# Performance work log

Measured on AMD Instinct MI355X. Metric: run time of the kernel, lower is better.

Reference implementation:

```python
import jax, jax.numpy as jnp
import numpy as np

T, B, C, H = 2048, 2, 1024, 16
D = C // H
SCALE = D ** -0.5
WSTD = C ** -0.5  # keep activations O(1) so softmax is not saturated


def setup_inputs() -> dict:
    key = jax.random.key(0)
    ks = jax.random.split(key, 6)
    return {
        "x": jax.random.normal(ks[0], (T, B, C), dtype=jnp.float32),
        "wq": jax.random.normal(ks[1], (C, C), dtype=jnp.float32) * WSTD,
        "wk": jax.random.normal(ks[2], (C, C), dtype=jnp.float32) * WSTD,
        "wv": jax.random.normal(ks[3], (C, C), dtype=jnp.float32) * WSTD,
        "wo": jax.random.normal(ks[4], (C, C), dtype=jnp.float32) * WSTD,
        "bo": jax.random.normal(ks[5], (C,), dtype=jnp.float32) * 0.02,
    }


def reference(x, wq, wk, wv, wo, bo):
    t, b, c = x.shape
    x2 = x.reshape(t * b, c)
    # SelfAttentionLinears: q scaled by head_dim^-0.5 inside the addmm
    q = (x2 @ wq) * SCALE
    k = x2 @ wk
    v = x2 @ wv
    # fairseq layout: (T, B*H, D) -> (B*H, T, D)
    q = q.reshape(t, b * H, D).transpose(1, 0, 2)
    k = k.reshape(t, b * H, D).transpose(1, 0, 2)
    v = v.reshape(t, b * H, D).transpose(1, 0, 2)
    # strided_bmm1: scores [B*H, T, T]
    scores = jnp.einsum('bqd,bkd->bqk', q, k)
    attn = jax.nn.softmax(scores, axis=-1)
    # strided_bmm2: context [B*H, T, D]
    ctx = jnp.einsum('bqk,bkd->bqd', attn, v)
    out = ctx.transpose(1, 0, 2).reshape(t, b, c)
    return out @ wo + bo
```

## Files before the change

kernel.cpp:

```cpp
#include <hip/hip_runtime.h>
#include <math.h>

#define T_DIM 2048
#define B_DIM 2
#define C_DIM 1024
#define H_DIM 16
#define D_DIM 64
#define M_DIM (T_DIM * B_DIM)
#define SCALE_QL2 0.18033688f

typedef short short8 __attribute__((ext_vector_type(8)));
typedef float f32x4  __attribute__((ext_vector_type(4)));
typedef unsigned short ushort_t;

__device__ __forceinline__ unsigned short f2bf(float f) {
    unsigned int u = __builtin_bit_cast(unsigned int, f);
    u += 0x7FFFu + ((u >> 16) & 1u);
    return (unsigned short)(u >> 16);
}

__device__ __forceinline__ void gl_lds16(const void* g, void* l) {
    __builtin_amdgcn_global_load_lds(
        (const __attribute__((address_space(1))) void*)g,
        (__attribute__((address_space(3))) void*)l, 16, 0, 0);
}

__global__ __launch_bounds__(256) void prep(
    const float* __restrict__ x,
    const float* __restrict__ wq, const float* __restrict__ wk,
    const float* __restrict__ wv, const float* __restrict__ wo,
    ushort_t* __restrict__ xb,
    ushort_t* __restrict__ wqkv_t, ushort_t* __restrict__ wo_t)
{
    __shared__ float tile[64][65];
    const int tid = threadIdx.x;
    const int z   = blockIdx.z;

    if (z == 4) {
        const size_t base =
            ((size_t)(blockIdx.y * 16 + blockIdx.x)) * 16384 + (size_t)tid * 8;
#pragma unroll
        for (int j = 0; j < 8; ++j) {
            const size_t i = base + (size_t)j * 2048;
            const float4 v0 = *(const float4*)&x[i];
            const float4 v1 = *(const float4*)&x[i + 4];
            ushort_t o[8] = {f2bf(v0.x), f2bf(v0.y), f2bf(v0.z), f2bf(v0.w),
                             f2bf(v1.x), f2bf(v1.y), f2bf(v1.z), f2bf(v1.w)};
            *(uint4*)&xb[i] = *(uint4*)o;
        }
        return;
    }

    const int k0 = blockIdx.x * 64;
    const int n0 = blockIdx.y * 64;
    const float* src = (z == 0) ? wq : (z == 1) ? wk : (z == 2) ? wv : wo;
    ushort_t* dst = (z < 3) ? (wqkv_t + (size_t)z * C_DIM * C_DIM) : wo_t;

    const int r = tid >> 4;
    const int c = (tid & 15) * 4;
#pragma unroll
    for (int i = 0; i < 4; ++i) {
        const float4 v = *(const float4*)&src[(size_t)(k0 + r + i * 16) * C_DIM + n0 + c];
        *(float4*)&tile[r + i * 16][c] = v;
    }
    __syncthreads();
#pragma unroll
    for (int i = 0; i < 4; ++i) {
        const int r2 = r + i * 16;
        ushort4 o;
        o.x = f2bf(tile[c + 0][r2]); o.y = f2bf(tile[c + 1][r2]);
        o.z = f2bf(tile[c + 2][r2]); o.w = f2bf(tile[c + 3][r2]);
        *(ushort4*)&dst[(size_t)(n0 + r2) * C_DIM + k0 + c] = o;
    }
}

__global__ __launch_bounds__(256) void qkv_mfma(
    const ushort_t* __restrict__ xb, const ushort_t* __restrict__ wt,
    ushort_t* __restrict__ q_ws, ushort_t* __restrict__ k_ws,
    ushort_t* __restrict__ v_ws)
{
    __shared__ ushort_t lds[18432];
    ushort_t* As = lds;
    ushort_t* Bs = lds + 4096;

    const int tid  = threadIdx.x;
    const int n0   = blockIdx.x * 128;
    const int m0   = blockIdx.y * 128;
    const int w    = tid >> 6;
    const int lane = tid & 63;
    const int l16  = lane & 15;
    const int quad = lane >> 4;
    const int wm   = (w >> 1) * 64;
    const int wn   = (w & 1) * 64;

    const int o0 = tid * 8, o1 = o0 + 2048;
    const ushort_t* a0 = xb + (size_t)(m0 + (o0 >> 5)) * C_DIM + (o0 & 31);
    const ushort_t* a1 = xb + (size_t)(m0 + (o1 >> 5)) * C_DIM + (o1 & 31);
    const ushort_t* b0 = wt + (size_t)(n0 + (o0 >> 5)) * C_DIM + (o0 & 31);
    const ushort_t* b1 = wt + (size_t)(n0 + (o1 >> 5)) * C_DIM + (o1 & 31);

    f32x4 acc[4][4] = {};

    for (int k0 = 0; k0 < C_DIM; k0 += 32) {
        __syncthreads();
        gl_lds16(a0 + k0, As + o0);
        gl_lds16(a1 + k0, As + o1);
        gl_lds16(b0 + k0, Bs + o0);
        gl_lds16(b1 + k0, Bs + o1);
        __syncthreads();

        short8 af[4], bf[4];
#pragma unroll
        for (int mi = 0; mi < 4; ++mi)
            af[mi] = *(const short8*)&As[(wm + mi * 16 + l16) * 32 + quad * 8];
#pragma unroll
        for (int ni = 0; ni < 4; ++ni)
            bf[ni] = *(const short8*)&Bs[(wn + ni * 16 + l16) * 32 + quad * 8];
#pragma unroll
        for (int mi = 0; mi < 4; ++mi)
#pragma unroll
            for (int ni = 0; ni < 4; ++ni)
                acc[mi][ni] = __builtin_amdgcn_mfma_f32_16x16x32_bf16(
                    af[mi], bf[ni], acc[mi][ni], 0, 0, 0);
    }

    __syncthreads();
    ushort_t* Ep = lds + w * 4608;

    const int mat = n0 >> 10;
    const int cb  = (n0 & 1023) + wn;
    const int h   = cb >> 6;
    ushort_t* dst = (mat == 0) ? q_ws : (mat == 1) ? k_ws : v_ws;
    const float sc = (mat == 0) ? SCALE_QL2 : 1.0f;

#pragma unroll
    for (int mi = 0; mi < 4; ++mi)
#pragma unroll
        for (int ni = 0; ni < 4; ++ni)
#pragma unroll
            for (int r = 0; r < 4; ++r)
                Ep[(mi * 16 + quad * 4 + r) * 72 + ni * 16 + l16] =
                    f2bf(acc[mi][ni][r] * sc);

    const int rq = lane >> 3;
    const int c8 = (lane & 7) * 8;
#pragma unroll
    for (int p = 0; p < 8; ++p) {
        const int row = p * 8 + rq;
        const uint4 val = *(const uint4*)&Ep[row * 72 + c8];
        const int m = m0 + wm + row;
        const int t = m >> 1, b = m & 1;
        *(uint4*)&dst[((size_t)(b * H_DIM + h) * T_DIM + t) * D_DIM + c8] = val;
    }
}

__global__ __launch_bounds__(256) void v_transpose(
    const ushort_t* __restrict__ vn, ushort_t* __restrict__ vt)
{
    __shared__ ushort_t tile[64][72];
    const int tid = threadIdx.x;
    const int t0  = blockIdx.x * 64;
    const int bh  = blockIdx.y;
    const int r   = tid >> 3;
    const int c   = (tid & 7) * 8;
#pragma unroll
    for (int i = 0; i < 2; ++i)
        *(uint4*)&tile[r + i * 32][c] =
            *(const uint4*)&vn[((size_t)bh * T_DIM + t0 + r + i * 32) * D_DIM + c];
    __syncthreads();
#pragma unroll
    for (int i = 0; i < 2; ++i) {
        const int rd = r + i * 32;
        ushort_t o[8];
#pragma unroll
        for (int j = 0; j < 8; ++j) o[j] = tile[c + j][rd];
        *(uint4*)&vt[((size_t)bh * D_DIM + rd) * T_DIM + t0 + c] = *(uint4*)o;
    }
}

__global__ __launch_bounds__(256) void attn_mfma(
    const ushort_t* __restrict__ q, const ushort_t* __restrict__ k,
    const ushort_t* __restrict__ v, ushort_t* __restrict__ ctx)
{
    __shared__ ushort_t Ks [64][72];
    __shared__ ushort_t Vts[64][72];
    __shared__ ushort_t Ps [64][72];

    const int tid  = threadIdx.x;
    const int bh   = blockIdx.x;
    const int q0   = blockIdx.y * 64;
    const int w    = tid >> 6;
    const int lane = tid & 63;
    const int l16  = lane & 15;
    const int quad = lane >> 4;

    const int r0 = tid >> 3,         c80 = (tid & 7) * 8;
    const int r1 = (tid + 256) >> 3;
    const ushort_t* kbase = k + (size_t)bh * T_DIM * D_DIM;
    const ushort_t* vbase = v + (size_t)bh * D_DIM * T_DIM;

    short8 aq0, aq1;
    {
        const ushort_t* qrow = q + ((size_t)bh * T_DIM + q0 + 16 * w + l16) * D_DIM;
        aq0 = *(const short8*)(qrow + quad * 8);
        aq1 = *(const short8*)(qrow + 32 + quad * 8);
    }

    short8 vones;
#pragma unroll
    for (int j = 0; j < 8; ++j) vones[j] = (short)0x3F80;

    f32x4 O[4] = {};
    f32x4 Osum = {};

    const ushort_t* kp0 = kbase + (size_t)r0 * D_DIM + c80;
    const ushort_t* kp1 = kbase + (size_t)r1 * D_DIM + c80;
    const ushort_t* vp0 = vbase + (size_t)r0 * T_DIM + c80;
    const ushort_t* vp1 = vbase + (size_t)r1 * T_DIM + c80;
    uint4 kr0 = *(const uint4*)kp0;  kp0 += 64 * D_DIM;
    uint4 kr1 = *(const uint4*)kp1;  kp1 += 64 * D_DIM;
    uint4 vr0 = *(const uint4*)vp0;  vp0 += 64;
    uint4 vr1 = *(const uint4*)vp1;  vp1 += 64;

    for (int kt = 0; kt < 32; ++kt) {
        __syncthreads();
        *(uint4*)&Ks[r0][c80]  = kr0;
        *(uint4*)&Ks[r1][c80]  = kr1;
        *(uint4*)&Vts[r0][c80] = vr0;
        *(uint4*)&Vts[r1][c80] = vr1;
        if (kt + 1 < 32) {
            kr0 = *(const uint4*)kp0;  kp0 += 64 * D_DIM;
            kr1 = *(const uint4*)kp1;  kp1 += 64 * D_DIM;
            vr0 = *(const uint4*)vp0;  vp0 += 64;
            vr1 = *(const uint4*)vp1;  vp1 += 64;
        }
        __syncthreads();

        f32x4 S[4];
        __builtin_amdgcn_s_setprio(1);
#pragma unroll
        for (int nt = 0; nt < 4; ++nt) {
            const short8 b0 = *(const short8*)&Ks[nt * 16 + l16][quad * 8];
            const short8 b1 = *(const short8*)&Ks[nt * 16 + l16][32 + quad * 8];
            f32x4 s = (f32x4){0.f, 0.f, 0.f, 0.f};
            s = __builtin_amdgcn_mfma_f32_16x16x32_bf16(aq0, b0, s, 0, 0, 0);
            s = __builtin_amdgcn_mfma_f32_16x16x32_bf16(aq1, b1, s, 0, 0, 0);
            S[nt] = s;
        }
        __builtin_amdgcn_s_setprio(0);

#pragma unroll
        for (int nt = 0; nt < 4; ++nt)
#pragma unroll
            for (int r = 0; r < 4; ++r) {
                union { float f; ushort2 h; } cv;
                cv.f = exp2f(S[nt][r]);
                Ps[16 * w + quad * 4 + r][nt * 16 + l16] = cv.h.y;
            }

        const short8 ap0 = *(const short8*)&Ps[16 * w + l16][quad * 8];
        const short8 ap1 = *(const short8*)&Ps[16 * w + l16][32 + quad * 8];

        __builtin_amdgcn_s_setprio(1);
        Osum = __builtin_amdgcn_mfma_f32_16x16x32_bf16(ap0, vones, Osum, 0, 0, 0);
        Osum = __builtin_amdgcn_mfma_f32_16x16x32_bf16(ap1, vones, Osum, 0, 0, 0);

#pragma unroll
        for (int nt = 0; nt < 4; ++nt) {
            const short8 b0 = *(const short8*)&Vts[nt * 16 + l16][quad * 8];
            const short8 b1 = *(const short8*)&Vts[nt * 16 + l16][32 + quad * 8];
            O[nt] = __builtin_amdgcn_mfma_f32_16x16x32_bf16(ap0, b0, O[nt], 0, 0, 0);
            O[nt] = __builtin_amdgcn_mfma_f32_16x16x32_bf16(ap1, b1, O[nt], 0, 0, 0);
        }
        __builtin_amdgcn_s_setprio(0);
    }

    const int b = bh >> 4;
    const int h = bh & 15;
#pragma unroll
    for (int r = 0; r < 4; ++r) {
        const float inv = 1.0f / Osum[r];
        const int row = q0 + 16 * w + quad * 4 + r;
#pragma unroll
        for (int nt = 0; nt < 4; ++nt)
            ctx[((size_t)row * B_DIM + b) * C_DIM + h * 64 + nt * 16 + l16] =
                f2bf(O[nt][r] * inv);
    }
}

__global__ __launch_bounds__(256) void out_mfma(
    const ushort_t* __restrict__ ctx, const ushort_t* __restrict__ wot,
    const float* __restrict__ bo, float* __restrict__ out)
{
    __shared__ ushort_t As[128 * 32];
    __shared__ ushort_t Bs[64 * 32];

    const int tid  = threadIdx.x;
    const int n0   = blockIdx.x * 64;
    const int m0   = blockIdx.y * 128;
    const int w    = tid >> 6;
    const int lane = tid & 63;
    const int l16  = lane & 15;
    const int quad = lane >> 4;
    const int wm   = (w >> 1) * 64;
    const int wn   = (w & 1) * 32;

    const int o0 = tid * 8, o1 = o0 + 2048;
    const ushort_t* a0 = ctx + (size_t)(m0 + (o0 >> 5)) * C_DIM + (o0 & 31);
    const ushort_t* a1 = ctx + (size_t)(m0 + (o1 >> 5)) * C_DIM + (o1 & 31);
    const ushort_t* b0 = wot + (size_t)(n0 + (o0 >> 5)) * C_DIM + (o0 & 31);

    f32x4 acc[4][2] = {};

    for (int k0 = 0; k0 < C_DIM; k0 += 32) {
        __syncthreads();
        gl_lds16(a0 + k0, As + o0);
        gl_lds16(a1 + k0, As + o1);
        gl_lds16(b0 + k0, Bs + o0);
        __syncthreads();

        short8 af[4], bf[2];
#pragma unroll
        for (int mi = 0; mi < 4; ++mi)
            af[mi] = *(const short8*)&As[(wm + mi * 16 + l16) * 32 + quad * 8];
#pragma unroll
        for (int ni = 0; ni < 2; ++ni)
            bf[ni] = *(const short8*)&Bs[(wn + ni * 16 + l16) * 32 + quad * 8];
#pragma unroll
        for (int mi = 0; mi < 4; ++mi)
#pragma unroll
            for (int ni = 0; ni < 2; ++ni)
                acc[mi][ni] = __builtin_amdgcn_mfma_f32_16x16x32_bf16(
                    af[mi], bf[ni], acc[mi][ni], 0, 0, 0);
    }

#pragma unroll
    for (int ni = 0; ni < 2; ++ni) {
        const int n = n0 + wn + ni * 16 + l16;
        const float bias = bo[n];
#pragma unroll
        for (int mi = 0; mi < 4; ++mi) {
            const int mb = m0 + wm + mi * 16 + quad * 4;
#pragma unroll
            for (int r = 0; r < 4; ++r)
                out[(size_t)(mb + r) * C_DIM + n] = acc[mi][ni][r] + bias;
        }
    }
}

extern "C" void kernel_launch(void* const* d_in, const int* in_sizes, int n_in,
                              void* d_out, int out_size, void* d_ws, size_t ws_size,
                              hipStream_t stream)
{
    const float* x  = (const float*)d_in[0];
    const float* wq = (const float*)d_in[1];
    const float* wk = (const float*)d_in[2];
    const float* wv = (const float*)d_in[3];
    const float* wo = (const float*)d_in[4];
    const float* bo = (const float*)d_in[5];
    float* out = (float*)d_out;

    const size_t CC  = (size_t)C_DIM * C_DIM;
    const size_t MC  = (size_t)M_DIM * C_DIM;
    ushort_t* xb     = (ushort_t*)d_ws;
    ushort_t* wqkv_t = xb + MC;
    ushort_t* wo_t   = wqkv_t + 3 * CC;
    ushort_t* q_ws   = wo_t + CC;
    ushort_t* k_ws   = q_ws + MC;
    ushort_t* v_nat  = k_ws + MC;
    ushort_t* v_t    = v_nat + MC;
    ushort_t* ctx    = v_t + MC;

    hipLaunchKernelGGL(prep, dim3(16, 16, 5), dim3(256), 0, stream,
                       x, wq, wk, wv, wo, xb, wqkv_t, wo_t);
    hipLaunchKernelGGL(qkv_mfma, dim3(24, 32), dim3(256), 0, stream,
                       xb, wqkv_t, q_ws, k_ws, v_nat);
    hipLaunchKernelGGL(v_transpose, dim3(32, 32), dim3(256), 0, stream,
                       v_nat, v_t);
    hipLaunchKernelGGL(attn_mfma, dim3(32, 32), dim3(256), 0, stream,
                       q_ws, k_ws, v_t, ctx);
    hipLaunchKernelGGL(out_mfma, dim3(16, 32), dim3(256), 0, stream,
                       ctx, wo_t, bo, out);
}
```

Baseline: 213.0 us.

## Switch attention to 32x32 MFMA with register-resident P via permlane swaps

Rewrites the attention kernel to use 32x32x16 bf16 MFMA. It computes S transposed (K as the A operand) so the exp'd probabilities can be repacked in registers with v_permlane32_swap instead of going through a shared-memory P tile. Each block now covers 128 query rows (32 per wave), which halves the grid and doubles K/V tile reuse. It also uses the hardware exp2 builtin. The cost is higher register pressure from the 16-wide accumulators and fewer blocks to fill the GPU.

```diff
diff --git a/kernel.cpp b/kernel.cpp
--- a/kernel.cpp
+++ b/kernel.cpp
@@ -9,9 +9,16 @@
 #define M_DIM (T_DIM * B_DIM)
 #define SCALE_QL2 0.18033688f
 
-typedef short short8 __attribute__((ext_vector_type(8)));
-typedef float f32x4  __attribute__((ext_vector_type(4)));
+typedef short short8  __attribute__((ext_vector_type(8)));
+typedef float f32x4   __attribute__((ext_vector_type(4)));
+typedef float f32x16  __attribute__((ext_vector_type(16)));
 typedef unsigned short ushort_t;
+
+#if __has_builtin(__builtin_amdgcn_exp2f)
+#define EXP2(x) __builtin_amdgcn_exp2f(x)
+#else
+#define EXP2(x) exp2f(x)
+#endif
 
 __device__ __forceinline__ unsigned short f2bf(float f) {
     unsigned int u = __builtin_bit_cast(unsigned int, f);
@@ -184,34 +191,35 @@
 {
     __shared__ ushort_t Ks [64][72];
     __shared__ ushort_t Vts[64][72];
-    __shared__ ushort_t Ps [64][72];
 
     const int tid  = threadIdx.x;
     const int bh   = blockIdx.x;
-    const int q0   = blockIdx.y * 64;
+    const int q0   = blockIdx.y * 128;
     const int w    = tid >> 6;
     const int lane = tid & 63;
-    const int l16  = lane & 15;
-    const int quad = lane >> 4;
+    const int l32  = lane & 31;
+    const int hi   = lane >> 5;
 
     const int r0 = tid >> 3,         c80 = (tid & 7) * 8;
-    const int r1 = (tid + 256) >> 3;
+    const int r1 = r0 + 32;
     const ushort_t* kbase = k + (size_t)bh * T_DIM * D_DIM;
     const ushort_t* vbase = v + (size_t)bh * D_DIM * T_DIM;
 
-    short8 aq0, aq1;
+    short8 qreg[4];
     {
-        const ushort_t* qrow = q + ((size_t)bh * T_DIM + q0 + 16 * w + l16) * D_DIM;
-        aq0 = *(const short8*)(qrow + quad * 8);
-        aq1 = *(const short8*)(qrow + 32 + quad * 8);
+        const ushort_t* qrow =
+            q + ((size_t)bh * T_DIM + q0 + 32 * w + l32) * D_DIM + hi * 8;
+#pragma unroll
+        for (int s = 0; s < 4; ++s)
+            qreg[s] = *(const short8*)(qrow + s * 16);
     }
 
     short8 vones;
 #pragma unroll
     for (int j = 0; j < 8; ++j) vones[j] = (short)0x3F80;
 
-    f32x4 O[4] = {};
-    f32x4 Osum = {};
+    f32x16 O0 = {}, O1 = {};
+    f32x16 Osum = {};
 
     const ushort_t* kp0 = kbase + (size_t)r0 * D_DIM + c80;
     const ushort_t* kp1 = kbase + (size_t)r1 * D_DIM + c80;
@@ -236,41 +244,58 @@
         }
         __syncthreads();
 
-        f32x4 S[4];
+        f32x16 st0 = {}, st1 = {};
         __builtin_amdgcn_s_setprio(1);
 #pragma unroll
-        for (int nt = 0; nt < 4; ++nt) {
-            const short8 b0 = *(const short8*)&Ks[nt * 16 + l16][quad * 8];
-            const short8 b1 = *(const short8*)&Ks[nt * 16 + l16][32 + quad * 8];
-            f32x4 s = (f32x4){0.f, 0.f, 0.f, 0.f};
-            s = __builtin_amdgcn_mfma_f32_16x16x32_bf16(aq0, b0, s, 0, 0, 0);
-            s = __builtin_amdgcn_mfma_f32_16x16x32_bf16(aq1, b1, s, 0, 0, 0);
-            S[nt] = s;
+        for (int s = 0; s < 4; ++s) {
+            const short8 ak0 = *(const short8*)&Ks[l32]     [s * 16 + hi * 8];
+            const short8 ak1 = *(const short8*)&Ks[32 + l32][s * 16 + hi * 8];
+            st0 = __builtin_amdgcn_mfma_f32_32x32x16_bf16(ak0, qreg[s], st0, 0, 0, 0);
+            st1 = __builtin_amdgcn_mfma_f32_32x32x16_bf16(ak1, qreg[s], st1, 0, 0, 0);
         }
         __builtin_amdgcn_s_setprio(0);
 
-#pragma unroll
-        for (int nt = 0; nt < 4; ++nt)
-#pragma unroll
-            for (int r = 0; r < 4; ++r) {
-                union { float f; ushort2 h; } cv;
-                cv.f = exp2f(S[nt][r]);
-                Ps[16 * w + quad * 4 + r][nt * 16 + l16] = cv.h.y;
-            }
-
-        const short8 ap0 = *(const short8*)&Ps[16 * w + l16][quad * 8];
-        const short8 ap1 = *(const short8*)&Ps[16 * w + l16][32 + quad * 8];
+        unsigned wpk0[8], wpk1[8];
+#pragma unroll
+        for (int i = 0; i < 8; ++i) {
+            const float a0 = EXP2(st0[2 * i]);
+            const float a1 = EXP2(st0[2 * i + 1]);
+            const float b0 = EXP2(st1[2 * i]);
+            const float b1 = EXP2(st1[2 * i + 1]);
+            wpk0[i] = __builtin_amdgcn_perm(
+                __builtin_bit_cast(unsigned, a1),
+                __builtin_bit_cast(unsigned, a0), 0x07060302u);
+            wpk1[i] = __builtin_amdgcn_perm(
+                __builtin_bit_cast(unsigned, b1),
+                __builtin_bit_cast(unsigned, b0), 0x07060302u);
+        }
+
+        short8 ap[4];
+#pragma unroll
+        for (int pr = 0; pr < 2; ++pr) {
+            unsigned x0 = wpk0[4 * pr + 0], y0 = wpk0[4 * pr + 2];
+            unsigned x1 = wpk0[4 * pr + 1], y1 = wpk0[4 * pr + 3];
+            asm("v_permlane32_swap_b32 %0, %1" : "+v"(x0), "+v"(y0));
+            asm("v_permlane32_swap_b32 %0, %1" : "+v"(x1), "+v"(y1));
+            uint4 fw = {x0, x1, y0, y1};
+            ap[pr] = __builtin_bit_cast(short8, fw);
+
+            unsigned u0 = wpk1[4 * pr + 0], z0 = wpk1[4 * pr + 2];
+            unsigned u1 = wpk1[4 * pr + 1], z1 = wpk1[4 * pr + 3];
+            asm("v_permlane32_swap_b32 %0, %1" : "+v"(u0), "+v"(z0));
+            asm("v_permlane32_swap_b32 %0, %1" : "+v"(u1), "+v"(z1));
+            uint4 fw1 = {u0, u1, z0, z1};
+            ap[2 + pr] = __builtin_bit_cast(short8, fw1);
+        }
 
         __builtin_amdgcn_s_setprio(1);
-        Osum = __builtin_amdgcn_mfma_f32_16x16x32_bf16(ap0, vones, Osum, 0, 0, 0);
-        Osum = __builtin_amdgcn_mfma_f32_16x16x32_bf16(ap1, vones, Osum, 0, 0, 0);
-
-#pragma unroll
-        for (int nt = 0; nt < 4; ++nt) {
-            const short8 b0 = *(const short8*)&Vts[nt * 16 + l16][quad * 8];
-            const short8 b1 = *(const short8*)&Vts[nt * 16 + l16][32 + quad * 8];
-            O[nt] = __builtin_amdgcn_mfma_f32_16x16x32_bf16(ap0, b0, O[nt], 0, 0, 0);
-            O[nt] = __builtin_amdgcn_mfma_f32_16x16x32_bf16(ap1, b1, O[nt], 0, 0, 0);
+#pragma unroll
+        for (int s = 0; s < 4; ++s) {
+            Osum = __builtin_amdgcn_mfma_f32_32x32x16_bf16(ap[s], vones, Osum, 0, 0, 0);
+            const short8 bv0 = *(const short8*)&Vts[l32]     [s * 16 + hi * 8];
+            const short8 bv1 = *(const short8*)&Vts[32 + l32][s * 16 + hi * 8];
+            O0 = __builtin_amdgcn_mfma_f32_32x32x16_bf16(ap[s], bv0, O0, 0, 0, 0);
+            O1 = __builtin_amdgcn_mfma_f32_32x32x16_bf16(ap[s], bv1, O1, 0, 0, 0);
         }
         __builtin_amdgcn_s_setprio(0);
     }
@@ -278,13 +303,13 @@
     const int b = bh >> 4;
     const int h = bh & 15;
 #pragma unroll
-    for (int r = 0; r < 4; ++r) {
-        const float inv = 1.0f / Osum[r];
-        const int row = q0 + 16 * w + quad * 4 + r;
-#pragma unroll
-        for (int nt = 0; nt < 4; ++nt)
-            ctx[((size_t)row * B_DIM + b) * C_DIM + h * 64 + nt * 16 + l16] =
-                f2bf(O[nt][r] * inv);
+    for (int reg = 0; reg < 16; ++reg) {
+        const int qrel = (reg & 3) + 8 * (reg >> 2) + 4 * hi;
+        const float inv = 1.0f / Osum[reg];
+        const int row = q0 + 32 * w + qrel;
+        const size_t base = ((size_t)row * B_DIM + b) * C_DIM + h * 64 + l32;
+        ctx[base]      = f2bf(O0[reg] * inv);
+        ctx[base + 32] = f2bf(O1[reg] * inv);
     }
 }
 
@@ -377,7 +402,7 @@
                        xb, wqkv_t, q_ws, k_ws, v_nat);
     hipLaunchKernelGGL(v_transpose, dim3(32, 32), dim3(256), 0, stream,
                        v_nat, v_t);
-    hipLaunchKernelGGL(attn_mfma, dim3(32, 32), dim3(256), 0, stream,
+    hipLaunchKernelGGL(attn_mfma, dim3(32, 16), dim3(256), 0, stream,
                        q_ws, k_ws, v_t, ctx);
     hipLaunchKernelGGL(out_mfma, dim3(16, 32), dim3(256), 0, stream,
                        ctx, wo_t, bo, out);
```

Measured after the change: 189.4 us. 1.12x faster.
